# Kernel optimization log

Measured on AMD Instinct MI355X. Metric: run time of the kernel, lower is better.

Reference implementation:

```python
import jax, jax.numpy as jnp
import numpy as np

VOCAB, EMB, HID = 50000, 256, 512
B, S = 64, 1024

def setup_inputs() -> dict:
    key = jax.random.key(0)
    ks = jax.random.split(key, 12)
    s = lambda k, shape, scale: jax.random.normal(k, shape, jnp.float32) * scale
    return {
        "x": jax.random.randint(ks[0], (B, S), 0, VOCAB, jnp.int32),
        "emb": s(ks[1], (VOCAB, EMB), 1.0),
        "Wxh0": s(ks[2], (EMB, HID), (1.0 / EMB) ** 0.5),
        "bxh0": s(ks[3], (HID,), 0.02),
        "Whh0": s(ks[4], (HID, HID), (1.0 / HID) ** 0.5),
        "bhh0": s(ks[5], (HID,), 0.02),
        "Wxh1": s(ks[6], (HID, HID), (1.0 / HID) ** 0.5),
        "bxh1": s(ks[7], (HID,), 0.02),
        "Whh1": s(ks[8], (HID, HID), (1.0 / HID) ** 0.5),
        "bhh1": s(ks[9], (HID,), 0.02),
        "fc_w": s(ks[10], (HID, 1), (1.0 / HID) ** 0.5),
        "fc_b": s(ks[11], (1,), 0.02),
    }

def reference(x, emb, Wxh0, bxh0, Whh0, bhh0, Wxh1, bxh1, Whh1, bhh1, fc_w, fc_b):
    # Embedding lookup: [B, S, EMB] -> time-major [S, B, EMB] for scan
    xe = jnp.swapaxes(emb[x], 0, 1)
    h0 = jnp.zeros((x.shape[0], Whh0.shape[0]), xe.dtype)
    h1 = jnp.zeros_like(h0)

    def step(carry, x_t):
        h0, h1 = carry
        h0 = jnp.tanh(x_t @ Wxh0 + bxh0 + h0 @ Whh0 + bhh0)  # layer 0
        h1 = jnp.tanh(h0 @ Wxh1 + bxh1 + h1 @ Whh1 + bhh1)   # layer 1
        return (h0, h1), None

    (h0, h1), _ = jax.lax.scan(step, (h0, h1), xe)
    return jax.nn.sigmoid(h1 @ fc_w + fc_b)  # [B, 1]
```

## Files before the change

kernel.cpp:

```cpp
#include <hip/hip_runtime.h>
#include <hip/hip_bf16.h>
#include <math.h>


typedef __bf16 bf16_t;
typedef __bf16 bf16x8 __attribute__((ext_vector_type(8)));
typedef float  floatx4 __attribute__((ext_vector_type(4)));
typedef unsigned int  u32;
typedef unsigned short u16;
typedef u32 u32x4 __attribute__((ext_vector_type(4)));

#define S_LEN  1024
#define BATCH  64
#define EMBD   256
#define HID    512
#define VOCAB  50000
#define D0     8
#define D1     4
#define NGROUP 4
#define NSLICE 8
#define NFLAGS (NGROUP * 64)
#define RING0_ELEMS ((size_t)D0*BATCH*HID)
#define RING1_ELEMS ((size_t)D1*BATCH*HID)
#define INIT_WORDS ((RING0_ELEMS + RING1_ELEMS)/2 + NFLAGS)

__device__ __attribute__((aligned(16)))  bf16_t g_h0ring[RING0_ELEMS];
__device__ __attribute__((aligned(16)))  bf16_t g_h1ring[RING1_ELEMS];
__device__ __attribute__((aligned(256))) int g_f2[NFLAGS];

__device__ __forceinline__ void at_store16(u16* p, u16 v) {
  __hip_atomic_store(p, v, __ATOMIC_RELAXED, __HIP_MEMORY_SCOPE_AGENT);
}
__device__ __forceinline__ void at_store32(u32* p, u32 v) {
  __hip_atomic_store(p, v, __ATOMIC_RELAXED, __HIP_MEMORY_SCOPE_AGENT);
}
__device__ __forceinline__ int at_loadi(const int* p) {
  return __hip_atomic_load(p, __ATOMIC_RELAXED, __HIP_MEMORY_SCOPE_AGENT);
}
__device__ __forceinline__ void at_storei(int* p, int v) {
  __hip_atomic_store(p, v, __ATOMIC_RELAXED, __HIP_MEMORY_SCOPE_AGENT);
}

__device__ __forceinline__ void wait_fused(const int* fg, int ta, int tc, int lane) {
  if (ta <= 0 && tc <= 0) return;
  const int* p = fg + lane;
  int tgt = (lane < 32) ? ta : tc;
  while (!__all(at_loadi(p) >= tgt)) __builtin_amdgcn_s_sleep(1);
}
__device__ __forceinline__ void wait_set(const int* fs, int tgt, int lane) {
  if (tgt <= 0) return;
  const int* p = fs + (lane & 31);
  while (!__all(at_loadi(p) >= tgt)) __builtin_amdgcn_s_sleep(1);
}

__device__ __forceinline__ floatx4 ring_gemm16(const bf16_t* hp,
                                               const bf16x8* bwf, floatx4 acc) {
  u32x4 rw[8];
#pragma unroll
  for (int ks = 0; ks < 8; ++ks)
    asm volatile("global_load_dwordx4 %0, %1, off offset:%2 sc0 sc1"
                 : "=v"(rw[ks]) : "v"(hp), "i"(ks * 64) : "memory");
  asm volatile("s_waitcnt vmcnt(0)" ::: "memory");
  __builtin_amdgcn_sched_barrier(0);
#pragma unroll
  for (int ks = 0; ks < 8; ++ks)
    acc = __builtin_amdgcn_mfma_f32_16x16x32_bf16(
        __builtin_bit_cast(bf16x8, rw[ks]), bwf[ks], acc, 0, 0, 0);
#pragma unroll
  for (int ks = 0; ks < 8; ++ks)
    asm volatile("global_load_dwordx4 %0, %1, off offset:%2 sc0 sc1"
                 : "=v"(rw[ks]) : "v"(hp), "i"(512 + ks * 64) : "memory");
  asm volatile("s_waitcnt vmcnt(0)" ::: "memory");
  __builtin_amdgcn_sched_barrier(0);
#pragma unroll
  for (int ks = 0; ks < 8; ++ks)
    acc = __builtin_amdgcn_mfma_f32_16x16x32_bf16(
        __builtin_bit_cast(bf16x8, rw[ks]), bwf[ks + 8], acc, 0, 0, 0);
  return acc;
}

__device__ __forceinline__ float act_tanh(float x) {
  x = fminf(fmaxf(x, -12.0f), 12.0f);
  float e = __expf(2.0f * x);
  return 1.0f - 2.0f / (e + 1.0f);
}

__device__ __forceinline__ bf16x8 load_bfrag(const float* __restrict__ W,
                                             int kbase, int col) {
  bf16x8 v;
#pragma unroll
  for (int j = 0; j < 8; ++j) v[j] = (bf16_t)W[(size_t)(kbase + j) * HID + col];
  return v;
}
__device__ __forceinline__ bf16x8 load_afrag(const float* __restrict__ p) {
  bf16x8 v;
#pragma unroll
  for (int j = 0; j < 8; ++j) v[j] = (bf16_t)p[j];
  return v;
}

__global__ __launch_bounds__(256) void k_init() {
  size_t i = (size_t)blockIdx.x * 256 + threadIdx.x;
  size_t r0w = RING0_ELEMS / 2, r1w = RING1_ELEMS / 2;
  if (i < r0w)             at_store32((u32*)g_h0ring + i, 0u);
  else if (i < r0w + r1w)  at_store32((u32*)g_h1ring + (i - r0w), 0u);
  else if (i < INIT_WORDS) at_store32((u32*)g_f2 + (i - r0w - r1w), 0u);
}

__global__ __launch_bounds__(256, 1) void k_rnn(
    const int* __restrict__ x,
    const float* __restrict__ emb,
    const float* __restrict__ Wxh0,
    const float* __restrict__ bxh0, const float* __restrict__ bhh0,
    const float* __restrict__ Whh0,
    const float* __restrict__ Wxh1,
    const float* __restrict__ bxh1, const float* __restrict__ bhh1,
    const float* __restrict__ Whh1) {
  int bid = blockIdx.x;
  int role = bid & 1, g = (bid >> 1) & 3, s = bid >> 3;
  int tid = threadIdx.x;
  int wv = tid >> 6, lane = tid & 63, l15 = lane & 15, quad = lane >> 4;
  int col = s * 64 + wv * 16 + l15;
  int arow = g * 16 + l15;
  int crow = g * 16 + quad * 4;
  int kb = quad * 8;
  int sw = s * 4 + wv;
  int* fg = g_f2 + g * 64;

  if (role == 0) {
    bf16x8 bw[16], bwx[8];
#pragma unroll
    for (int ks = 0; ks < 16; ++ks) bw[ks]  = load_bfrag(Whh0, ks * 32 + kb, col);
#pragma unroll
    for (int ks = 0; ks < 8;  ++ks) bwx[ks] = load_bfrag(Wxh0, ks * 32 + kb, col);
    float bb = bxh0[col] + bhh0[col];

    int xrow = arow * S_LEN;
    bf16x8 ea[8], en[8];
    {
      int xi0 = x[xrow];
      xi0 = xi0 < 0 ? 0 : (xi0 >= VOCAB ? VOCAB - 1 : xi0);
      const float* ep = emb + (size_t)xi0 * EMBD + kb;
#pragma unroll
      for (int ks = 0; ks < 8; ++ks) ea[ks] = load_afrag(ep + ks * 32);
    }
    int xiB = x[xrow + 1];

    for (int t = 0; t < S_LEN; ++t) {
      if (t + 1 < S_LEN) {
        int xi = xiB < 0 ? 0 : (xiB >= VOCAB ? VOCAB - 1 : xiB);
        const float* ep = emb + (size_t)xi * EMBD + kb;
#pragma unroll
        for (int ks = 0; ks < 8; ++ks) en[ks] = load_afrag(ep + ks * 32);
      }
      int tn = (t + 2 < S_LEN) ? t + 2 : S_LEN - 1;
      int xiC = x[xrow + tn];

      floatx4 acc = (floatx4){bb, bb, bb, bb};
#pragma unroll
      for (int ks = 0; ks < 8; ++ks)
        acc = __builtin_amdgcn_mfma_f32_16x16x32_bf16(ea[ks], bwx[ks], acc, 0, 0, 0);

      wait_fused(fg, t, t - D0 + 1, lane);

      if (t > 0) {
        const bf16_t* hp = g_h0ring + (size_t)((t - 1) % D0) * BATCH * HID
                         + (size_t)arow * HID + kb;
        acc = ring_gemm16(hp, bw, acc);
      }
      bf16_t* hw = g_h0ring + (size_t)(t % D0) * BATCH * HID
                 + (size_t)crow * HID + col;
#pragma unroll
      for (int i = 0; i < 4; ++i) {
        bf16_t hv = (bf16_t)act_tanh(acc[i]);
        at_store16((u16*)(hw + i * HID), __builtin_bit_cast(u16, hv));
      }

      asm volatile("s_waitcnt vmcnt(0)" ::: "memory");
      if (lane == 0) at_storei(&fg[sw], t + 1);
#pragma unroll
      for (int ks = 0; ks < 8; ++ks) ea[ks] = en[ks];
      xiB = xiC;
    }
  } else {
    bf16x8 bwx[16], bwh[16];
#pragma unroll
    for (int ks = 0; ks < 16; ++ks) {
      bwx[ks] = load_bfrag(Wxh1, ks * 32 + kb, col);
      bwh[ks] = load_bfrag(Whh1, ks * 32 + kb, col);
    }
    float bb = bxh1[col] + bhh1[col];

    for (int t = 0; t < S_LEN; ++t) {
      wait_set(fg + 32, t, lane);

      floatx4 acc = (floatx4){bb, bb, bb, bb};
      if (t > 0) {
        const bf16_t* hp = g_h1ring + (size_t)((t - 1) % D1) * BATCH * HID
                         + (size_t)arow * HID + kb;
        acc = ring_gemm16(hp, bwh, acc);
      }

      wait_set(fg, t + 1, lane);
      {
        const bf16_t* hp = g_h0ring + (size_t)(t % D0) * BATCH * HID
                         + (size_t)arow * HID + kb;
        acc = ring_gemm16(hp, bwx, acc);
      }
      bf16_t* hw = g_h1ring + (size_t)(t % D1) * BATCH * HID
                 + (size_t)crow * HID + col;
#pragma unroll
      for (int i = 0; i < 4; ++i) {
        bf16_t hv = (bf16_t)act_tanh(acc[i]);
        at_store16((u16*)(hw + i * HID), __builtin_bit_cast(u16, hv));
      }

      asm volatile("s_waitcnt vmcnt(0)" ::: "memory");
      if (lane == 0) at_storei(&fg[32 + sw], t + 1);
    }
  }
}

__global__ __launch_bounds__(64) void k_out(const float* __restrict__ fc_w,
                                            const float* __restrict__ fc_b,
                                            float* __restrict__ out) {
  int b = threadIdx.x;
  const bf16_t* hr = g_h1ring + (size_t)((S_LEN - 1) % D1) * BATCH * HID
                   + (size_t)b * HID;
  float acc = fc_b[0];
  for (int c = 0; c < HID; c += 64) {
    u32x4 rw[8];
#pragma unroll
    for (int i = 0; i < 8; ++i)
      asm volatile("global_load_dwordx4 %0, %1, off offset:%2 sc0 sc1"
                   : "=v"(rw[i]) : "v"(hr + c), "i"(i * 16) : "memory");
    asm volatile("s_waitcnt vmcnt(0)" ::: "memory");
    __builtin_amdgcn_sched_barrier(0);
#pragma unroll
    for (int i = 0; i < 8; ++i) {
      bf16x8 h = __builtin_bit_cast(bf16x8, rw[i]);
#pragma unroll
      for (int j = 0; j < 8; ++j)
        acc += (float)h[j] * fc_w[c + i * 8 + j];
    }
  }
  acc = fminf(fmaxf(acc, -30.0f), 30.0f);
  out[b] = 1.0f / (1.0f + __expf(-acc));
}

extern "C" void kernel_launch(void* const* d_in, const int* in_sizes, int n_in,
                              void* d_out, int out_size, void* d_ws, size_t ws_size,
                              hipStream_t stream) {
  const int*   x    = (const int*)d_in[0];
  const float* emb  = (const float*)d_in[1];
  const float* Wxh0 = (const float*)d_in[2];
  const float* bxh0 = (const float*)d_in[3];
  const float* Whh0 = (const float*)d_in[4];
  const float* bhh0 = (const float*)d_in[5];
  const float* Wxh1 = (const float*)d_in[6];
  const float* bxh1 = (const float*)d_in[7];
  const float* Whh1 = (const float*)d_in[8];
  const float* bhh1 = (const float*)d_in[9];
  const float* fc_w = (const float*)d_in[10];
  const float* fc_b = (const float*)d_in[11];
  (void)d_ws; (void)ws_size; (void)in_sizes; (void)n_in; (void)out_size;

  hipLaunchKernelGGL(k_init, dim3((INIT_WORDS + 255) / 256), dim3(256), 0, stream);
  hipLaunchKernelGGL(k_rnn, dim3(NGROUP * 2 * NSLICE), dim3(256), 0, stream,
                     x, emb, Wxh0, bxh0, bhh0, Whh0, Wxh1, bxh1, bhh1, Whh1);
  hipLaunchKernelGGL(k_out, dim3(1), dim3(64), 0, stream,
                     fc_w, fc_b, (float*)d_out);
}
```

Before: 6.444 ms.

## Batch recurrent ring loads per step and split MFMA accumulators

Each layer now issues all hidden-state ring loads for a step at once with a single wait, instead of two or four serialized load-then-wait rounds. Layer 1 also waits on both flag sets in one fused poll before loading both rings. MFMAs are split across two independent accumulators to shorten the dependent chain. The embedding prefetch for the next step moves after the flag store, which may put its load latency before the next step's input MFMAs. The t=0 special case is removed and relies on the rings starting zeroed.

```diff
diff --git a/kernel.cpp b/kernel.cpp
--- a/kernel.cpp
+++ b/kernel.cpp
@@ -46,37 +46,6 @@
   const int* p = fg + lane;
   int tgt = (lane < 32) ? ta : tc;
   while (!__all(at_loadi(p) >= tgt)) __builtin_amdgcn_s_sleep(1);
-}
-__device__ __forceinline__ void wait_set(const int* fs, int tgt, int lane) {
-  if (tgt <= 0) return;
-  const int* p = fs + (lane & 31);
-  while (!__all(at_loadi(p) >= tgt)) __builtin_amdgcn_s_sleep(1);
-}
-
-__device__ __forceinline__ floatx4 ring_gemm16(const bf16_t* hp,
-                                               const bf16x8* bwf, floatx4 acc) {
-  u32x4 rw[8];
-#pragma unroll
-  for (int ks = 0; ks < 8; ++ks)
-    asm volatile("global_load_dwordx4 %0, %1, off offset:%2 sc0 sc1"
-                 : "=v"(rw[ks]) : "v"(hp), "i"(ks * 64) : "memory");
-  asm volatile("s_waitcnt vmcnt(0)" ::: "memory");
-  __builtin_amdgcn_sched_barrier(0);
-#pragma unroll
-  for (int ks = 0; ks < 8; ++ks)
-    acc = __builtin_amdgcn_mfma_f32_16x16x32_bf16(
-        __builtin_bit_cast(bf16x8, rw[ks]), bwf[ks], acc, 0, 0, 0);
-#pragma unroll
-  for (int ks = 0; ks < 8; ++ks)
-    asm volatile("global_load_dwordx4 %0, %1, off offset:%2 sc0 sc1"
-                 : "=v"(rw[ks]) : "v"(hp), "i"(512 + ks * 64) : "memory");
-  asm volatile("s_waitcnt vmcnt(0)" ::: "memory");
-  __builtin_amdgcn_sched_barrier(0);
-#pragma unroll
-  for (int ks = 0; ks < 8; ++ks)
-    acc = __builtin_amdgcn_mfma_f32_16x16x32_bf16(
-        __builtin_bit_cast(bf16x8, rw[ks]), bwf[ks + 8], acc, 0, 0, 0);
-  return acc;
 }
 
 __device__ __forceinline__ float act_tanh(float x) {
@@ -136,7 +105,7 @@
     float bb = bxh0[col] + bhh0[col];
 
     int xrow = arow * S_LEN;
-    bf16x8 ea[8], en[8];
+    bf16x8 ea[8];
     {
       int xi0 = x[xrow];
       xi0 = xi0 < 0 ? 0 : (xi0 >= VOCAB ? VOCAB - 1 : xi0);
@@ -146,41 +115,53 @@
     }
     int xiB = x[xrow + 1];
 
+#pragma unroll 1
     for (int t = 0; t < S_LEN; ++t) {
+      floatx4 acc0 = (floatx4){bb, bb, bb, bb};
+#pragma unroll
+      for (int ks = 0; ks < 8; ++ks)
+        acc0 = __builtin_amdgcn_mfma_f32_16x16x32_bf16(ea[ks], bwx[ks], acc0, 0, 0, 0);
+
+      wait_fused(fg, t, t - D0 + 1, lane);
+
+      const bf16_t* hp = g_h0ring + (size_t)((t + D0 - 1) % D0) * BATCH * HID
+                       + (size_t)arow * HID + kb;
+      u32x4 rw[16];
+#pragma unroll
+      for (int ks = 0; ks < 16; ++ks)
+        asm volatile("global_load_dwordx4 %0, %1, off offset:%2 sc0 sc1"
+                     : "=v"(rw[ks]) : "v"(hp), "i"(ks * 64) : "memory");
+      asm volatile("s_waitcnt vmcnt(0)" ::: "memory");
+      __builtin_amdgcn_sched_barrier(0);
+
+      floatx4 acc1 = (floatx4){0.f, 0.f, 0.f, 0.f};
+#pragma unroll
+      for (int ks = 0; ks < 8; ++ks) {
+        acc0 = __builtin_amdgcn_mfma_f32_16x16x32_bf16(
+            __builtin_bit_cast(bf16x8, rw[2 * ks]),     bw[2 * ks],     acc0, 0, 0, 0);
+        acc1 = __builtin_amdgcn_mfma_f32_16x16x32_bf16(
+            __builtin_bit_cast(bf16x8, rw[2 * ks + 1]), bw[2 * ks + 1], acc1, 0, 0, 0);
+      }
+
+      bf16_t* hw = g_h0ring + (size_t)(t % D0) * BATCH * HID
+                 + (size_t)crow * HID + col;
+#pragma unroll
+      for (int i = 0; i < 4; ++i) {
+        bf16_t hv = (bf16_t)act_tanh(acc0[i] + acc1[i]);
+        at_store16((u16*)(hw + i * HID), __builtin_bit_cast(u16, hv));
+      }
+
+      asm volatile("s_waitcnt vmcnt(0)" ::: "memory");
+      if (lane == 0) at_storei(&fg[sw], t + 1);
+
       if (t + 1 < S_LEN) {
         int xi = xiB < 0 ? 0 : (xiB >= VOCAB ? VOCAB - 1 : xiB);
         const float* ep = emb + (size_t)xi * EMBD + kb;
 #pragma unroll
-        for (int ks = 0; ks < 8; ++ks) en[ks] = load_afrag(ep + ks * 32);
-      }
-      int tn = (t + 2 < S_LEN) ? t + 2 : S_LEN - 1;
-      int xiC = x[xrow + tn];
-
-      floatx4 acc = (floatx4){bb, bb, bb, bb};
-#pragma unroll
-      for (int ks = 0; ks < 8; ++ks)
-        acc = __builtin_amdgcn_mfma_f32_16x16x32_bf16(ea[ks], bwx[ks], acc, 0, 0, 0);
-
-      wait_fused(fg, t, t - D0 + 1, lane);
-
-      if (t > 0) {
-        const bf16_t* hp = g_h0ring + (size_t)((t - 1) % D0) * BATCH * HID
-                         + (size_t)arow * HID + kb;
-        acc = ring_gemm16(hp, bw, acc);
-      }
-      bf16_t* hw = g_h0ring + (size_t)(t % D0) * BATCH * HID
-                 + (size_t)crow * HID + col;
-#pragma unroll
-      for (int i = 0; i < 4; ++i) {
-        bf16_t hv = (bf16_t)act_tanh(acc[i]);
-        at_store16((u16*)(hw + i * HID), __builtin_bit_cast(u16, hv));
-      }
-
-      asm volatile("s_waitcnt vmcnt(0)" ::: "memory");
-      if (lane == 0) at_storei(&fg[sw], t + 1);
-#pragma unroll
-      for (int ks = 0; ks < 8; ++ks) ea[ks] = en[ks];
-      xiB = xiC;
+        for (int ks = 0; ks < 8; ++ks) ea[ks] = load_afrag(ep + ks * 32);
+        int tn = (t + 2 < S_LEN) ? t + 2 : S_LEN - 1;
+        xiB = x[xrow + tn];
+      }
     }
   } else {
     bf16x8 bwx[16], bwh[16];
@@ -191,27 +172,41 @@
     }
     float bb = bxh1[col] + bhh1[col];
 
+#pragma unroll 1
     for (int t = 0; t < S_LEN; ++t) {
-      wait_set(fg + 32, t, lane);
-
-      floatx4 acc = (floatx4){bb, bb, bb, bb};
-      if (t > 0) {
-        const bf16_t* hp = g_h1ring + (size_t)((t - 1) % D1) * BATCH * HID
-                         + (size_t)arow * HID + kb;
-        acc = ring_gemm16(hp, bwh, acc);
-      }
-
-      wait_set(fg, t + 1, lane);
-      {
-        const bf16_t* hp = g_h0ring + (size_t)(t % D0) * BATCH * HID
-                         + (size_t)arow * HID + kb;
-        acc = ring_gemm16(hp, bwx, acc);
-      }
+      wait_fused(fg, t + 1, t, lane);
+
+      const bf16_t* hp0 = g_h0ring + (size_t)(t % D0) * BATCH * HID
+                        + (size_t)arow * HID + kb;
+      const bf16_t* hp1 = g_h1ring + (size_t)((t + D1 - 1) % D1) * BATCH * HID
+                        + (size_t)arow * HID + kb;
+      u32x4 rw0[16], rw1[16];
+#pragma unroll
+      for (int ks = 0; ks < 16; ++ks)
+        asm volatile("global_load_dwordx4 %0, %1, off offset:%2 sc0 sc1"
+                     : "=v"(rw0[ks]) : "v"(hp0), "i"(ks * 64) : "memory");
+#pragma unroll
+      for (int ks = 0; ks < 16; ++ks)
+        asm volatile("global_load_dwordx4 %0, %1, off offset:%2 sc0 sc1"
+                     : "=v"(rw1[ks]) : "v"(hp1), "i"(ks * 64) : "memory");
+      asm volatile("s_waitcnt vmcnt(0)" ::: "memory");
+      __builtin_amdgcn_sched_barrier(0);
+
+      floatx4 acc0 = (floatx4){bb, bb, bb, bb};
+      floatx4 acc1 = (floatx4){0.f, 0.f, 0.f, 0.f};
+#pragma unroll
+      for (int ks = 0; ks < 16; ++ks) {
+        acc0 = __builtin_amdgcn_mfma_f32_16x16x32_bf16(
+            __builtin_bit_cast(bf16x8, rw0[ks]), bwx[ks], acc0, 0, 0, 0);
+        acc1 = __builtin_amdgcn_mfma_f32_16x16x32_bf16(
+            __builtin_bit_cast(bf16x8, rw1[ks]), bwh[ks], acc1, 0, 0, 0);
+      }
+
       bf16_t* hw = g_h1ring + (size_t)(t % D1) * BATCH * HID
                  + (size_t)crow * HID + col;
 #pragma unroll
       for (int i = 0; i < 4; ++i) {
-        bf16_t hv = (bf16_t)act_tanh(acc[i]);
+        bf16_t hv = (bf16_t)act_tanh(acc0[i] + acc1[i]);
         at_store16((u16*)(hw + i * HID), __builtin_bit_cast(u16, hv));
       }
 
@@ -228,16 +223,17 @@
   const bf16_t* hr = g_h1ring + (size_t)((S_LEN - 1) % D1) * BATCH * HID
                    + (size_t)b * HID;
   float acc = fc_b[0];
-  for (int c = 0; c < HID; c += 64) {
-    u32x4 rw[8];
-#pragma unroll
-    for (int i = 0; i < 8; ++i)
+#pragma unroll 1
+  for (int c = 0; c < HID; c += 128) {
+    u32x4 rw[16];
+#pragma unroll
+    for (int i = 0; i < 16; ++i)
       asm volatile("global_load_dwordx4 %0, %1, off offset:%2 sc0 sc1"
                    : "=v"(rw[i]) : "v"(hr + c), "i"(i * 16) : "memory");
     asm volatile("s_waitcnt vmcnt(0)" ::: "memory");
     __builtin_amdgcn_sched_barrier(0);
 #pragma unroll
-    for (int i = 0; i < 8; ++i) {
+    for (int i = 0; i < 16; ++i) {
       bf16x8 h = __builtin_bit_cast(bf16x8, rw[i]);
 #pragma unroll
       for (int j = 0; j < 8; ++j)
```

New measurement: 5.956 ms. 7.6% less time.
